# Kernel tuning notes

Hardware: AMD Instinct MI355X
Metric: run time of the kernel (lower is better)

The kernel has to match this reference:

```python
import jax, jax.numpy as jnp
import numpy as np


def _conv(x, w, pad):
    # NCHW conv, stride 1
    return jax.lax.conv_general_dilated(
        x, w, (1, 1), [(pad, pad), (pad, pad)],
        dimension_numbers=('NCHW', 'OIHW', 'NCHW'))


def _bn_relu(x, s, b, m, v):
    # eval-mode BatchNorm2d (running stats) + ReLU, eps=1e-5
    inv = s / jnp.sqrt(v + 1e-5)
    return jax.nn.relu(x * inv[None, :, None, None] + (b - m * inv)[None, :, None, None])


def _pam(x, qw, qb, kw, kb, vw, vb, gamma):
    B, C, H, W = x.shape
    N = H * W
    q = (_conv(x, qw, 0) + qb[None, :, None, None]).reshape(B, -1, N)  # [B,Cr,N]
    k = (_conv(x, kw, 0) + kb[None, :, None, None]).reshape(B, -1, N)  # [B,Cr,N]
    v = (_conv(x, vw, 0) + vb[None, :, None, None]).reshape(B, C, N)   # [B,C,N]
    energy = jnp.einsum('bcn,bcm->bnm', q, k)          # [B,N,N], query n over keys m
    att = jax.nn.softmax(energy, axis=-1)
    out = jnp.einsum('bcm,bnm->bcn', v, att).reshape(B, C, H, W)
    return gamma * out + x


def _cam(x, gamma):
    B, C, H, W = x.shape
    f = x.reshape(B, C, -1)                            # [B,C,N]
    energy = jnp.einsum('bcn,bdn->bcd', f, f)          # [B,C,C]
    energy_new = jnp.max(energy, axis=-1, keepdims=True) - energy
    att = jax.nn.softmax(energy_new, axis=-1)
    out = jnp.einsum('bcd,bdn->bcn', att, f).reshape(B, C, H, W)
    return gamma * out + x


def _forward(x, w5a, bn5a_s, bn5a_b, bn5a_m, bn5a_v,
             pq_w, pq_b, pk_w, pk_b, pv_w, pv_b, p_gamma,
             w51, bn51_s, bn51_b, bn51_m, bn51_v,
             w5c, bn5c_s, bn5c_b, bn5c_m, bn5c_v, c_gamma,
             w52, bn52_s, bn52_b, bn52_m, bn52_v,
             w8, b8):
    feat1 = _bn_relu(_conv(x, w5a, 1), bn5a_s, bn5a_b, bn5a_m, bn5a_v)
    sa_feat = _pam(feat1, pq_w, pq_b, pk_w, pk_b, pv_w, pv_b, p_gamma)
    sa_conv = _bn_relu(_conv(sa_feat, w51, 1), bn51_s, bn51_b, bn51_m, bn51_v)
    feat2 = _bn_relu(_conv(x, w5c, 1), bn5c_s, bn5c_b, bn5c_m, bn5c_v)
    sc_feat = _cam(feat2, c_gamma)
    sc_conv = _bn_relu(_conv(sc_feat, w52, 1), bn52_s, bn52_b, bn52_m, bn52_v)
    feat_sum = sa_conv + sc_conv
    # conv8 = Dropout2d (identity in eval) -> 1x1 conv -> ReLU
    sasc = jax.nn.relu(_conv(feat_sum, w8, 0) + b8[None, :, None, None])
    return sasc


def setup_inputs() -> dict:
    key = jax.random.key(0)
    ks = iter(jax.random.split(key, 48))
    def rn(shape, scale=0.1):
        return jax.random.normal(next(ks), shape, jnp.float32) * scale
    def bn_params(c):
        s = rn((c,), 0.2) + 1.0
        b = rn((c,), 0.1)
        m = rn((c,), 0.1)
        v = jnp.abs(rn((c,), 0.5)) + 0.5
        return s, b, m, v
    Cin, Ci, Cout = 512, 32, 2
    Cr = max(1, Ci // 8)  # = 4
    inp = {}
    inp['x'] = jax.random.normal(next(ks), (4, Cin, 64, 64), jnp.float32)
    inp['w5a'] = rn((Ci, Cin, 3, 3), 0.05)
    inp['bn5a_s'], inp['bn5a_b'], inp['bn5a_m'], inp['bn5a_v'] = bn_params(Ci)
    inp['pq_w'] = rn((Cr, Ci, 1, 1)); inp['pq_b'] = rn((Cr,), 0.01)
    inp['pk_w'] = rn((Cr, Ci, 1, 1)); inp['pk_b'] = rn((Cr,), 0.01)
    inp['pv_w'] = rn((Ci, Ci, 1, 1)); inp['pv_b'] = rn((Ci,), 0.01)
    inp['p_gamma'] = jnp.full((1,), 0.5, jnp.float32)
    inp['w51'] = rn((Ci, Ci, 3, 3))
    inp['bn51_s'], inp['bn51_b'], inp['bn51_m'], inp['bn51_v'] = bn_params(Ci)
    inp['w5c'] = rn((Ci, Cin, 3, 3), 0.05)
    inp['bn5c_s'], inp['bn5c_b'], inp['bn5c_m'], inp['bn5c_v'] = bn_params(Ci)
    inp['c_gamma'] = jnp.full((1,), 0.5, jnp.float32)
    inp['w52'] = rn((Ci, Ci, 3, 3))
    inp['bn52_s'], inp['bn52_b'], inp['bn52_m'], inp['bn52_v'] = bn_params(Ci)
    inp['w8'] = rn((Cout, Ci, 1, 1)); inp['b8'] = rn((Cout,), 0.01)
    return inp


def reference(x, w5a, bn5a_s, bn5a_b, bn5a_m, bn5a_v,
              pq_w, pq_b, pk_w, pk_b, pv_w, pv_b, p_gamma,
              w51, bn51_s, bn51_b, bn51_m, bn51_v,
              w5c, bn5c_s, bn5c_b, bn5c_m, bn5c_v, c_gamma,
              w52, bn52_s, bn52_b, bn52_m, bn52_v,
              w8, b8):
    return _forward(x, w5a, bn5a_s, bn5a_b, bn5a_m, bn5a_v,
                    pq_w, pq_b, pk_w, pk_b, pv_w, pv_b, p_gamma,
                    w51, bn51_s, bn51_b, bn51_m, bn51_v,
                    w5c, bn5c_s, bn5c_b, bn5c_m, bn5c_v, c_gamma,
                    w52, bn52_s, bn52_b, bn52_m, bn52_v,
                    w8, b8)
```

## Files before the change

kernel.cpp:

```cpp
#include <hip/hip_runtime.h>
#include <hip/hip_bf16.h>


typedef __attribute__((ext_vector_type(8))) short bf16x8;
typedef __attribute__((ext_vector_type(4))) float f32x4;

#define O_WPK   0
#define O_W51P  147456
#define O_W52P  152064
#define O_BNA   156672
#define O_W8    156928
#define O_PQW   157000
#define O_PKW   157132
#define O_PVW   157264
#define O_GAM   158320
#define O_Q     158400
#define O_K     223936
#define O_ENE   453312
#define O_PE    457408
#define O_F1T   985792
#define O_F2T   1510080
#define O_V     2034368
#define O_SAT   2558656
#define O_SCT   2837440
#define O_XT    461504
#define O_CP    4922048
#define O_PO    4922048
#define O_PS    3116224

__device__ __forceinline__ unsigned short f2b(float f){
  __hip_bfloat16 h = __float2bfloat16(f);
  return *(unsigned short*)&h;
}

__global__ __launch_bounds__(256) void k_prep_all(
  const float* w5a, const float* w5c,
  const float* w51, const float* w52,
  const float* s0,const float* b0,const float* m0,const float* v0,
  const float* s1,const float* b1,const float* m1,const float* v1,
  const float* s2,const float* b2,const float* m2,const float* v2,
  const float* s3,const float* b3,const float* m3,const float* v3,
  const float* w8,const float* b8,
  const float* pqw,const float* pqb,const float* pkw,const float* pkb,
  const float* pvw,const float* pvb,const float* pg,const float* cg,
  float* ws)
{
  int bx = blockIdx.x;
  int tid = threadIdx.x;
  if (bx < 1152){
    int id = bx*256 + tid;
    int tap = id >> 15;
    int r = id & 32767;
    int cb = r >> 11;
    int r2 = r & 2047;
    int co = r2 >> 5, ci = r2 & 31;
    int cin = cb*32 + ci;
    float v = (co < 32) ? w5a[co*4608 + cin*9 + tap] : w5c[(co-32)*4608 + cin*9 + tap];
    ((unsigned short*)ws)[id] = f2b(v);
    return;
  }
  if (bx < 1231){
    int id = (bx-1152)*256 + tid;
    if (id >= 20076) return;
    if (id < 9216){ int tap=id>>10, co=(id>>5)&31, ci=id&31;
      ((unsigned short*)(ws + O_W51P))[id] = f2b(w51[co*288 + ci*9 + tap]); return; }
    id -= 9216;
    if (id < 9216){ int tap=id>>10, co=(id>>5)&31, ci=id&31;
      ((unsigned short*)(ws + O_W52P))[id] = f2b(w52[co*288 + ci*9 + tap]); return; }
    id -= 9216;
    if (id < 256){
      int conv = id>>6, ab = (id>>5)&1, c = id&31;
      const float *S,*Bb,*M,*V;
      if (conv==0){S=s0;Bb=b0;M=m0;V=v0;} else if (conv==1){S=s1;Bb=b1;M=m1;V=v1;}
      else if (conv==2){S=s2;Bb=b2;M=m2;V=v2;} else {S=s3;Bb=b3;M=m3;V=v3;}
      float A = S[c] * rsqrtf(V[c] + 1e-5f);
      ws[O_BNA + conv*64 + ab*32 + c] = ab ? (Bb[c] - M[c]*A) : A;
      return; }
    id -= 256;
    if (id < 64){ ws[O_W8+id] = w8[id]; return; } id -= 64;
    if (id < 2){ ws[O_W8+64+id] = b8[id]; return; } id -= 2;
    if (id < 128){ ws[O_PQW+id] = pqw[id]; return; } id -= 128;
    if (id < 4){ ws[O_PQW+128+id] = pqb[id]; return; } id -= 4;
    if (id < 128){ ws[O_PKW+id] = pkw[id]; return; } id -= 128;
    if (id < 4){ ws[O_PKW+128+id] = pkb[id]; return; } id -= 4;
    if (id < 1024){ ws[O_PVW+id] = pvw[id]; return; } id -= 1024;
    if (id < 32){ ws[O_PVW+1024+id] = pvb[id]; return; } id -= 32;
    ws[O_GAM+id] = id ? cg[0] : pg[0];
    return;
  }
  {
    int i = (bx-1231)*256 + tid;
    if (i >= 66560) return;
    int part = i & 3; int j = i >> 2;
    int rp = j % 260; int bc = j / 260;
    int py, px;
    if (rp < 66){ py = 0; px = rp; }
    else if (rp < 132){ py = 65; px = rp - 66; }
    else if (rp < 196){ py = rp - 131; px = 0; }
    else { py = rp - 195; px = 65; }
    size_t off = (((size_t)bc*66 + py)*66 + px)*32 + part*8;
    *(uint4*)((unsigned short*)(ws + O_XT) + off) = make_uint4(0,0,0,0);
  }
}

__global__ __launch_bounds__(256) void k_nhwc(const float* __restrict__ x, float* __restrict__ ws){
  int y = blockIdx.x, ct = blockIdx.y, b = blockIdx.z;
  __shared__ unsigned short t16[64][65];
  int tid = threadIdx.x;
  int r0 = tid >> 4, c0 = (tid & 15) * 4;
  const float* xb = x + ((size_t)(b*512 + ct*64))*4096 + y*64;
  #pragma unroll
  for (int i = 0; i < 4; ++i){
    int row = r0 + i*16;
    float4 v = *(const float4*)(xb + (size_t)row*4096 + c0);
    t16[row][c0+0] = f2b(v.x);
    t16[row][c0+1] = f2b(v.y);
    t16[row][c0+2] = f2b(v.z);
    t16[row][c0+3] = f2b(v.w);
  }
  __syncthreads();
  int pixl = tid >> 2, q = tid & 3;
  unsigned short vs[16];
  #pragma unroll
  for (int j = 0; j < 16; ++j) vs[j] = t16[q*16 + j][pixl];
  unsigned u[8];
  #pragma unroll
  for (int j = 0; j < 8; ++j) u[j] = (unsigned)vs[2*j] | ((unsigned)vs[2*j+1] << 16);
  unsigned short* xt = (unsigned short*)(ws + O_XT);
  int cbl = ct*2 + (q>>1);
  size_t off = (((size_t)(b*16 + cbl)*66 + (y+1))*66 + (pixl+1))*32 + (q&1)*16;
  *(uint4*)(xt + off)     = make_uint4(u[0],u[1],u[2],u[3]);
  *(uint4*)(xt + off + 8) = make_uint4(u[4],u[5],u[6],u[7]);
}

__global__ __launch_bounds__(256) void k_conv_mfma(float* __restrict__ ws){
  int mb = blockIdx.x;
  int ks = blockIdx.y;
  int b = mb >> 6, y = mb & 63;
  __shared__ unsigned short Bs[198*40];
  int tid = threadIdx.x;
  int w = tid >> 6, l = tid & 63;
  f32x4 zero = {0.f,0.f,0.f,0.f};
  f32x4 acc[4] = {zero, zero, zero, zero};
  const unsigned short* wp = (const unsigned short*)ws;
  const unsigned short* xt = (const unsigned short*)(ws + O_XT);
  int arow = w*16 + (l & 15);
  int kq = (l >> 4)*8;
  int i0 = tid, i1 = tid + 256, i2 = tid + 512, i3 = tid + 768;
  const unsigned short* slab0 = xt + ((size_t)((b*16 + ks*4)*66 + y))*2112;
  uint4 r0 = *(const uint4*)(slab0 + i0*8);
  uint4 r1 = *(const uint4*)(slab0 + i1*8);
  uint4 r2 = *(const uint4*)(slab0 + i2*8);
  uint4 r3 = (tid < 24) ? *(const uint4*)(slab0 + i3*8) : make_uint4(0,0,0,0);
  for (int cb4 = 0; cb4 < 4; ++cb4){
    int cb = ks*4 + cb4;
    __syncthreads();
    *(uint4*)&Bs[(i0>>2)*40 + (i0&3)*8] = r0;
    *(uint4*)&Bs[(i1>>2)*40 + (i1&3)*8] = r1;
    *(uint4*)&Bs[(i2>>2)*40 + (i2&3)*8] = r2;
    if (tid < 24) *(uint4*)&Bs[(i3>>2)*40 + (i3&3)*8] = r3;
    __syncthreads();
    if (cb4 < 3){
      const unsigned short* slab = xt + ((size_t)((b*16 + cb + 1)*66 + y))*2112;
      r0 = *(const uint4*)(slab + i0*8);
      r1 = *(const uint4*)(slab + i1*8);
      r2 = *(const uint4*)(slab + i2*8);
      if (tid < 24) r3 = *(const uint4*)(slab + i3*8);
    }
    #pragma unroll
    for (int tap = 0; tap < 9; ++tap){
      int dy = tap/3, dx = tap - dy*3;
      bf16x8 af = *(const bf16x8*)(wp + (size_t)(tap*16 + cb)*2048 + arow*32 + kq);
      #pragma unroll
      for (int pt = 0; pt < 4; ++pt){
        int pix = pt*16 + (l&15) + dx;
        bf16x8 bv = *(const bf16x8*)&Bs[(dy*66 + pix)*40 + kq];
        acc[pt] = __builtin_amdgcn_mfma_f32_16x16x32_bf16(af, bv, acc[pt], 0, 0, 0);
      }
    }
  }
  float* cp = ws + O_CP + ((size_t)(ks*4 + b))*262144;
  int co0 = w*16 + (l>>4)*4;
  #pragma unroll
  for (int pt = 0; pt < 4; ++pt){
    int pix = y*64 + pt*16 + (l & 15);
    *(f32x4*)&cp[(size_t)pix*64 + co0] = acc[pt];
  }
}

__global__ __launch_bounds__(256) void k_reduce_feat(float* __restrict__ ws){
  int bx = blockIdx.x;
  if (bx < 4096){
    int id = bx*256 + threadIdx.x;
    float s = (ws[O_CP + id] + ws[O_CP + 1048576 + id])
            + (ws[O_CP + 2097152 + id] + ws[O_CP + 3145728 + id]);
    int co = id & 63; int rest = id >> 6;
    int conv = co >> 5, c = co & 31;
    float A = ws[O_BNA + conv*64 + c], Bb = ws[O_BNA + conv*64 + 32 + c];
    float val = fmaxf(A*s + Bb, 0.f);
    if (conv == 0) ws[O_F1T + (size_t)rest*32 + c] = val;
    else           ws[O_F2T + (size_t)rest*32 + c] = val;
    return;
  }
  {
    int i = (bx-4096)*256 + threadIdx.x;
    if (i >= 8320) return;
    int part = i & 3; int j = i >> 2;
    int arr = j / 1040; int rem = j - arr*1040;
    int b = rem / 260; int rp = rem % 260;
    int py, px;
    if (rp < 66){ py = 0; px = rp; }
    else if (rp < 132){ py = 65; px = rp - 66; }
    else if (rp < 196){ py = rp - 131; px = 0; }
    else { py = rp - 195; px = 65; }
    size_t off = (((size_t)(b*66) + py)*66 + px)*32 + part*8;
    unsigned short* base = (unsigned short*)(ws + O_SAT + arr*278784);
    *(uint4*)(base + off) = make_uint4(0,0,0,0);
  }
}

__global__ __launch_bounds__(256) void k_qkv_came(float* __restrict__ ws){
  int bx = blockIdx.x;
  int tid = threadIdx.x;
  __shared__ float wq[32], wk[32], wv[8][32];
  __shared__ float Fs[64*32];
  if (bx < 256){
    int id = bx*256 + tid;
    int part = id >> 14;
    int nid = id & 16383;
    int b = nid >> 12, n = nid & 4095;
    if (tid < 32){ wq[tid] = ws[O_PQW + part*32 + tid]; wk[tid] = ws[O_PKW + part*32 + tid]; }
    wv[tid>>5][tid&31] = ws[O_PVW + (part*8 + (tid>>5))*32 + (tid&31)];
    __syncthreads();
    const float* fp = ws + O_F1T + (size_t)nid*32;
    float fv[32];
    #pragma unroll
    for (int j=0;j<8;j++){
      float4 v = *(const float4*)(fp + j*4);
      fv[j*4]=v.x; fv[j*4+1]=v.y; fv[j*4+2]=v.z; fv[j*4+3]=v.w;
    }
    float q = ws[O_PQW+128+part], k = ws[O_PKW+128+part];
    #pragma unroll
    for (int c=0;c<32;c++){ q += wq[c]*fv[c]; k += wk[c]*fv[c]; }
    ws[O_Q + (((b<<2)+part)<<12) + n] = q;
    ws[O_K + (((b<<2)+part)<<12) + n] = k;
    unsigned short* vbp = (unsigned short*)(ws + O_V);
    #pragma unroll
    for (int j2=0;j2<8;j2++){
      int c2 = part*8 + j2;
      float v = ws[O_PVW+1024+c2];
      #pragma unroll
      for (int c=0;c<32;c++) v += wv[j2][c]*fv[c];
      vbp[(((b<<5)+c2)<<12) + n] = f2b(v);
    }
    return;
  }
  {
    int blk = bx - 256; int b = blk >> 6, ch = blk & 63;
    const float* f = ws + O_F2T + ((size_t)b<<17) + (size_t)ch*2048;
    for (int i = tid; i < 512; i += 256)
      *(float4*)&Fs[i*4] = *(const float4*)(f + i*4);
    __syncthreads();
    int c = tid >> 3, d0 = (tid & 7) * 4;
    float a0=0.f, a1=0.f, a2=0.f, a3=0.f;
    #pragma unroll 8
    for (int n = 0; n < 64; ++n){
      float fc = Fs[n*32 + c];
      float4 fd = *(const float4*)&Fs[n*32 + d0];
      a0 = fmaf(fc, fd.x, a0); a1 = fmaf(fc, fd.y, a1);
      a2 = fmaf(fc, fd.z, a2); a3 = fmaf(fc, fd.w, a3);
    }
    float* pe = ws + O_PE + ((size_t)(b*64 + ch))*1024;
    *(float4*)&pe[c*32 + d0] = make_float4(a0, a1, a2, a3);
  }
}

__global__ __launch_bounds__(256, 6) void k_pam_flash(float* __restrict__ ws){
  int nt = blockIdx.x;
  int b  = blockIdx.y;
  int ms = blockIdx.z;
  __shared__ float Ks[2][4][4][32];
  __shared__ float Ss[4][32];
  __shared__ float Os[4][32][36];
  int tid = threadIdx.x;
  int w = tid >> 6, l = tid & 63;
  int nn = l & 15, g = l >> 4;
  int n0 = (nt<<5) + nn;
  const float LOG2E = 1.44269504f;
  const float BIAS  = -28.8539008f;
  float q0[4], q1[4];
  #pragma unroll
  for (int cr=0;cr<4;++cr){
    q0[cr] = ws[O_Q + (((b<<2)+cr)<<12) + n0] * LOG2E;
    q1[cr] = ws[O_Q + (((b<<2)+cr)<<12) + n0 + 16] * LOG2E;
  }
  int e0i = l*2, cr_s = e0i >> 5, mm_s = e0i & 31;
  int mbase = ms*1024 + w*256;
  const float* ksrc = ws + O_K + (((b<<2)+cr_s)<<12) + mbase + mm_s;
  const unsigned short* vb = (const unsigned short*)(ws + O_V);
  int mo = g*8;
  const unsigned short* vp0 = vb + (((b<<5) + nn)<<12) + mbase + mo;
  const unsigned short* vp1 = vb + (((b<<5) + 16 + nn)<<12) + mbase + mo;
  f32x4 zero = {0.f,0.f,0.f,0.f};
  f32x4 acc00 = zero, acc01 = zero, acc10 = zero, acc11 = zero;
  float lsum0 = 0.f, lsum1 = 0.f;
  bf16x8 a0A = *(const bf16x8*)(vp0);
  bf16x8 a1A = *(const bf16x8*)(vp1);
  float2 kreg = *(const float2*)(ksrc);
  *(float2*)&Ks[0][w][cr_s][mm_s] = kreg;
  bf16x8 a0B, a1B;
  for (int ch = 0; ch < 8; ++ch){
    int buf = ch & 1;
    if (ch < 7){
      int mn = (ch+1)*32;
      a0B = *(const bf16x8*)(vp0 + mn);
      a1B = *(const bf16x8*)(vp1 + mn);
      kreg = *(const float2*)(ksrc + mn);
    }
    float e0[8], e1[8];
    {
      float4 ka, kb;
      ka = *(const float4*)&Ks[buf][w][0][mo];
      kb = *(const float4*)&Ks[buf][w][0][mo+4];
      e0[0]=fmaf(q0[0],ka.x,BIAS); e0[1]=fmaf(q0[0],ka.y,BIAS); e0[2]=fmaf(q0[0],ka.z,BIAS); e0[3]=fmaf(q0[0],ka.w,BIAS);
      e0[4]=fmaf(q0[0],kb.x,BIAS); e0[5]=fmaf(q0[0],kb.y,BIAS); e0[6]=fmaf(q0[0],kb.z,BIAS); e0[7]=fmaf(q0[0],kb.w,BIAS);
      e1[0]=fmaf(q1[0],ka.x,BIAS); e1[1]=fmaf(q1[0],ka.y,BIAS); e1[2]=fmaf(q1[0],ka.z,BIAS); e1[3]=fmaf(q1[0],ka.w,BIAS);
      e1[4]=fmaf(q1[0],kb.x,BIAS); e1[5]=fmaf(q1[0],kb.y,BIAS); e1[6]=fmaf(q1[0],kb.z,BIAS); e1[7]=fmaf(q1[0],kb.w,BIAS);
#define KACC(CR) \
      ka = *(const float4*)&Ks[buf][w][CR][mo]; \
      kb = *(const float4*)&Ks[buf][w][CR][mo+4]; \
      e0[0]=fmaf(q0[CR],ka.x,e0[0]); e0[1]=fmaf(q0[CR],ka.y,e0[1]); e0[2]=fmaf(q0[CR],ka.z,e0[2]); e0[3]=fmaf(q0[CR],ka.w,e0[3]); \
      e0[4]=fmaf(q0[CR],kb.x,e0[4]); e0[5]=fmaf(q0[CR],kb.y,e0[5]); e0[6]=fmaf(q0[CR],kb.z,e0[6]); e0[7]=fmaf(q0[CR],kb.w,e0[7]); \
      e1[0]=fmaf(q1[CR],ka.x,e1[0]); e1[1]=fmaf(q1[CR],ka.y,e1[1]); e1[2]=fmaf(q1[CR],ka.z,e1[2]); e1[3]=fmaf(q1[CR],ka.w,e1[3]); \
      e1[4]=fmaf(q1[CR],kb.x,e1[4]); e1[5]=fmaf(q1[CR],kb.y,e1[5]); e1[6]=fmaf(q1[CR],kb.z,e1[6]); e1[7]=fmaf(q1[CR],kb.w,e1[7]);
      KACC(1)
      KACC(2)
      KACC(3)
#undef KACC
    }
    union { bf16x8 v; unsigned short u[8]; } pb0, pb1;
    #pragma unroll
    for (int j=0;j<8;j++){ float p = __builtin_amdgcn_exp2f(e0[j]); lsum0 += p; pb0.u[j] = f2b(p); }
    #pragma unroll
    for (int j=0;j<8;j++){ float p = __builtin_amdgcn_exp2f(e1[j]); lsum1 += p; pb1.u[j] = f2b(p); }
    acc00 = __builtin_amdgcn_mfma_f32_16x16x32_bf16(a0A, pb0.v, acc00, 0, 0, 0);
    acc01 = __builtin_amdgcn_mfma_f32_16x16x32_bf16(a1A, pb0.v, acc01, 0, 0, 0);
    acc10 = __builtin_amdgcn_mfma_f32_16x16x32_bf16(a0A, pb1.v, acc10, 0, 0, 0);
    acc11 = __builtin_amdgcn_mfma_f32_16x16x32_bf16(a1A, pb1.v, acc11, 0, 0, 0);
    if (ch < 7){
      int nb = buf ^ 1;
      *(float2*)&Ks[nb][w][cr_s][mm_s] = kreg;
      a0A = a0B; a1A = a1B;
    }
  }
  lsum0 += __shfl_xor(lsum0, 16); lsum0 += __shfl_xor(lsum0, 32);
  lsum1 += __shfl_xor(lsum1, 16); lsum1 += __shfl_xor(lsum1, 32);
  if (l < 16){ Ss[w][l] = lsum0; Ss[w][16+l] = lsum1; }
  #pragma unroll
  for (int r=0;r<4;r++){
    Os[w][nn][g*4 + r]         = acc00[r];
    Os[w][nn][16 + g*4 + r]    = acc01[r];
    Os[w][16+nn][g*4 + r]      = acc10[r];
    Os[w][16+nn][16 + g*4 + r] = acc11[r];
  }
  __syncthreads();
  float* PO = ws + O_PO + (size_t)(ms*4+b)*131072 + nt*1024;
  for (int i = tid; i < 1024; i += 256){
    int nn2 = i >> 5, c = i & 31;
    PO[i] = Os[0][nn2][c] + Os[1][nn2][c] + Os[2][nn2][c] + Os[3][nn2][c];
  }
  if (tid < 32)
    ws[O_PS + (ms*4+b)*4096 + (nt<<5) + tid] = Ss[0][tid]+Ss[1][tid]+Ss[2][tid]+Ss[3][tid];
}

__global__ __launch_bounds__(256) void k_finred(float* __restrict__ ws){
  int bx = blockIdx.x;
  if (bx < 2048){
    int id = bx*256 + threadIdx.x;
    int c = id & 31;
    int n = (id >> 5) & 4095;
    int b = id >> 17;
    int pbase = (b*4096 + n)*32 + c;
    int sbase = b*4096 + n;
    float O = ws[O_PO + pbase] + ws[O_PO + 524288 + pbase]
            + ws[O_PO + 1048576 + pbase] + ws[O_PO + 1572864 + pbase];
    float S = ws[O_PS + sbase] + ws[O_PS + 16384 + sbase]
            + ws[O_PS + 32768 + sbase] + ws[O_PS + 49152 + sbase];
    float sa = ws[O_GAM]*(O/S) + ws[O_F1T + id];
    int y = n >> 6, xx = n & 63;
    ((unsigned short*)(ws + O_SAT))[(((size_t)((b*66 + y+1)*66 + xx+1))<<5) + c] = f2b(sa);
    return;
  }
  {
    int id = (bx-2048)*256 + threadIdx.x;
    int b = id >> 10, i = id & 1023;
    const float* pe = ws + O_PE + ((size_t)b<<16) + i;
    float s = 0.f;
    #pragma unroll 8
    for (int chk = 0; chk < 64; ++chk) s += pe[chk*1024];
    ws[O_ENE + id] = s;
  }
}

__global__ __launch_bounds__(256) void k_cam_out(float* __restrict__ ws){
  int blk = blockIdx.x;
  int b = blk >> 5;
  int chunk = blk & 31;
  int tid = threadIdx.x;
  int half = tid >> 7;
  int nl = tid & 127;
  int n = (chunk << 7) + nl;
  __shared__ float att[32][33];
  if (tid < 32){
    int c = tid;
    const float* e = ws + O_ENE + (b<<10) + (c<<5);
    float M = -1e30f, mn = 1e30f;
    #pragma unroll
    for (int d=0;d<32;d++){ M = fmaxf(M, e[d]); mn = fminf(mn, e[d]); }
    float mx2 = M - mn;
    float s = 0.f, ex[32];
    #pragma unroll
    for (int d=0;d<32;d++){ ex[d] = __expf((M - e[d]) - mx2); s += ex[d]; }
    float inv = 1.f/s;
    #pragma unroll
    for (int d=0;d<32;d++) att[c][d] = ex[d]*inv;
  }
  __syncthreads();
  const float* fp = ws + O_F2T + (((size_t)b<<12) + n)*32;
  float fv[32];
  #pragma unroll
  for (int j=0;j<8;j++){
    float4 v = *(const float4*)(fp + j*4);
    fv[j*4]=v.x; fv[j*4+1]=v.y; fv[j*4+2]=v.z; fv[j*4+3]=v.w;
  }
  float g = ws[O_GAM+1];
  int c0 = half*16;
  unsigned u[8];
  #pragma unroll
  for (int cp=0; cp<8; ++cp){
    int ca = c0 + 2*cp, cb = ca + 1;
    float o0 = 0.f, o1 = 0.f;
    #pragma unroll
    for (int d=0;d<32;d++){ o0 += att[ca][d]*fv[d]; o1 += att[cb][d]*fv[d]; }
    float r0 = g*o0 + fv[ca], r1 = g*o1 + fv[cb];
    u[cp] = (unsigned)f2b(r0) | ((unsigned)f2b(r1) << 16);
  }
  int y = n >> 6, xcol = n & 63;
  unsigned short* sct = (unsigned short*)(ws + O_SCT);
  size_t base = ((size_t)((b*66 + y+1)*66 + xcol+1))*32 + c0;
  *(uint4*)(sct + base)     = make_uint4(u[0],u[1],u[2],u[3]);
  *(uint4*)(sct + base + 8) = make_uint4(u[4],u[5],u[6],u[7]);
}

__global__ __launch_bounds__(256) void k_final_mfma(float* __restrict__ ws, float* __restrict__ out){
  int y = blockIdx.x, b = blockIdx.y;
  __shared__ unsigned short Bs[2*3*66*40];
  __shared__ float ep[2][2][2][16];
  int tid = threadIdx.x;
  int w = tid >> 6, l = tid & 63;
  int g = l >> 4, col = l & 15;
  const unsigned short* sat = (const unsigned short*)(ws + O_SAT);
  const unsigned short* sct = (const unsigned short*)(ws + O_SCT);
  for (int i = tid; i < 1584; i += 256){
    int row = i >> 2, part = i & 3;
    int conv = row / 198; int rr = row - conv*198;
    int dy = rr / 66; int pix = rr - dy*66;
    const unsigned short* src = (conv ? sct : sat) + ((size_t)((b*66 + y + dy)*66 + pix))*32 + part*8;
    *(uint4*)&Bs[(size_t)row*40 + part*8] = *(const uint4*)src;
  }
  __syncthreads();
  int cohalf = w & 1, ptbase = (w >> 1) * 2;
  const unsigned short* wp[2] = { (const unsigned short*)(ws + O_W51P), (const unsigned short*)(ws + O_W52P) };
  f32x4 zero = {0.f,0.f,0.f,0.f};
  f32x4 acc[2][2] = {{zero,zero},{zero,zero}};
  for (int dy = 0; dy < 3; ++dy){
    for (int dx = 0; dx < 3; ++dx){
      int tap = dy*3 + dx;
      #pragma unroll
      for (int conv = 0; conv < 2; ++conv){
        bf16x8 af = *(const bf16x8*)(wp[conv] + tap*1024 + (cohalf*16 + col)*32 + g*8);
        #pragma unroll
        for (int pt = 0; pt < 2; ++pt){
          int pix = (ptbase + pt)*16 + col + dx;
          bf16x8 bv = *(const bf16x8*)&Bs[(size_t)((conv*3 + dy)*66 + pix)*40 + g*8];
          acc[conv][pt] = __builtin_amdgcn_mfma_f32_16x16x32_bf16(af, bv, acc[conv][pt], 0, 0, 0);
        }
      }
    }
  }
  float p0[2], p1[2];
  #pragma unroll
  for (int pt = 0; pt < 2; ++pt){
    float s0 = 0.f, s1 = 0.f;
    #pragma unroll
    for (int r = 0; r < 4; ++r){
      int co = cohalf*16 + g*4 + r;
      float A1 = ws[O_BNA + 2*64 + co], B1 = ws[O_BNA + 2*64 + 32 + co];
      float A2 = ws[O_BNA + 3*64 + co], B2 = ws[O_BNA + 3*64 + 32 + co];
      float fs = fmaxf(A1*acc[0][pt][r] + B1, 0.f) + fmaxf(A2*acc[1][pt][r] + B2, 0.f);
      s0 += ws[O_W8 + co]*fs;
      s1 += ws[O_W8 + 32 + co]*fs;
    }
    s0 += __shfl_xor(s0, 16); s0 += __shfl_xor(s0, 32);
    s1 += __shfl_xor(s1, 16); s1 += __shfl_xor(s1, 32);
    p0[pt] = s0; p1[pt] = s1;
  }
  if (cohalf == 0 && l < 16){
    #pragma unroll
    for (int pt = 0; pt < 2; ++pt){ ep[w>>1][pt][0][l] = p0[pt]; ep[w>>1][pt][1][l] = p1[pt]; }
  }
  __syncthreads();
  if (cohalf == 1 && l < 16){
    float b80 = ws[O_W8 + 64], b81 = ws[O_W8 + 65];
    #pragma unroll
    for (int pt = 0; pt < 2; ++pt){
      int pix = y*64 + (w>>1)*32 + pt*16 + l;
      float o0 = p0[pt] + ep[w>>1][pt][0][l] + b80;
      float o1 = p1[pt] + ep[w>>1][pt][1][l] + b81;
      out[((b*2+0)<<12) + pix] = fmaxf(o0, 0.f);
      out[((b*2+1)<<12) + pix] = fmaxf(o1, 0.f);
    }
  }
}

extern "C" void kernel_launch(void* const* d_in, const int* in_sizes, int n_in,
                              void* d_out, int out_size, void* d_ws, size_t ws_size,
                              hipStream_t stream) {
  const float* x    = (const float*)d_in[0];
  float* ws = (float*)d_ws;
  float* out = (float*)d_out;

  k_prep_all<<<1491, 256, 0, stream>>>(
      (const float*)d_in[1], (const float*)d_in[18],
      (const float*)d_in[13], (const float*)d_in[24],
      (const float*)d_in[2],(const float*)d_in[3],(const float*)d_in[4],(const float*)d_in[5],
      (const float*)d_in[19],(const float*)d_in[20],(const float*)d_in[21],(const float*)d_in[22],
      (const float*)d_in[14],(const float*)d_in[15],(const float*)d_in[16],(const float*)d_in[17],
      (const float*)d_in[25],(const float*)d_in[26],(const float*)d_in[27],(const float*)d_in[28],
      (const float*)d_in[29],(const float*)d_in[30],
      (const float*)d_in[6],(const float*)d_in[7],(const float*)d_in[8],(const float*)d_in[9],
      (const float*)d_in[10],(const float*)d_in[11],(const float*)d_in[12],(const float*)d_in[23],
      ws);
  k_nhwc<<<dim3(64,8,4), 256, 0, stream>>>(x, ws);
  k_conv_mfma<<<dim3(256,4), 256, 0, stream>>>(ws);
  k_reduce_feat<<<4129, 256, 0, stream>>>(ws);
  k_qkv_came<<<512, 256, 0, stream>>>(ws);
  k_pam_flash<<<dim3(128,4,4), 256, 0, stream>>>(ws);
  k_finred<<<2064, 256, 0, stream>>>(ws);
  k_cam_out<<<128, 256, 0, stream>>>(ws);
  k_final_mfma<<<dim3(64,4), 256, 0, stream>>>(ws, out);
}
```

Measured before the change: 96.73 us.

## Fuse NHWC transpose into prep, and fuse split-K reduce with QKV and CAM energy

Merges the input NHWC/bf16 transpose into the weight-prep kernel, which saves one launch. Fuses the split-K conv reduction and BN+ReLU with the PAM q/k/v projection and the CAM Gram-matrix partials, all computed from a shared-memory tile, so the separate QKV/CAM kernel and its re-read of the features go away. It also vectorizes the final PAM reduction with f32x4 loads and packed bf16 stores. The costs are a larger partial-energy buffer (128 chunks instead of 64) and lower occupancy in the fused kernel because only half its threads do the projection.

```diff
diff --git a/kernel.cpp b/kernel.cpp
--- a/kernel.cpp
+++ b/kernel.cpp
@@ -17,7 +17,6 @@
 #define O_Q     158400
 #define O_K     223936
 #define O_ENE   453312
-#define O_PE    457408
 #define O_F1T   985792
 #define O_F2T   1510080
 #define O_V     2034368
@@ -27,13 +26,15 @@
 #define O_CP    4922048
 #define O_PO    4922048
 #define O_PS    3116224
+#define O_PE2   9437184
 
 __device__ __forceinline__ unsigned short f2b(float f){
   __hip_bfloat16 h = __float2bfloat16(f);
   return *(unsigned short*)&h;
 }
 
-__global__ __launch_bounds__(256) void k_prep_all(
+__global__ __launch_bounds__(256) void k_prep_nhwc(
+  const float* __restrict__ x,
   const float* w5a, const float* w5c,
   const float* w51, const float* w52,
   const float* s0,const float* b0,const float* m0,const float* v0,
@@ -47,8 +48,38 @@
 {
   int bx = blockIdx.x;
   int tid = threadIdx.x;
-  if (bx < 1152){
-    int id = bx*256 + tid;
+  __shared__ unsigned short t16[64][65];
+  if (bx < 2048){
+    int y = bx & 63, ct = (bx >> 6) & 7, b = bx >> 9;
+    int r0 = tid >> 4, c0 = (tid & 15) * 4;
+    const float* xb = x + ((size_t)(b*512 + ct*64))*4096 + y*64;
+    #pragma unroll
+    for (int i = 0; i < 4; ++i){
+      int row = r0 + i*16;
+      float4 v = *(const float4*)(xb + (size_t)row*4096 + c0);
+      t16[row][c0+0] = f2b(v.x);
+      t16[row][c0+1] = f2b(v.y);
+      t16[row][c0+2] = f2b(v.z);
+      t16[row][c0+3] = f2b(v.w);
+    }
+    __syncthreads();
+    int pixl = tid >> 2, q = tid & 3;
+    unsigned short vs[16];
+    #pragma unroll
+    for (int j = 0; j < 16; ++j) vs[j] = t16[q*16 + j][pixl];
+    unsigned u[8];
+    #pragma unroll
+    for (int j = 0; j < 8; ++j) u[j] = (unsigned)vs[2*j] | ((unsigned)vs[2*j+1] << 16);
+    unsigned short* xt = (unsigned short*)(ws + O_XT);
+    int cbl = ct*2 + (q>>1);
+    size_t off = (((size_t)(b*16 + cbl)*66 + (y+1))*66 + (pixl+1))*32 + (q&1)*16;
+    *(uint4*)(xt + off)     = make_uint4(u[0],u[1],u[2],u[3]);
+    *(uint4*)(xt + off + 8) = make_uint4(u[4],u[5],u[6],u[7]);
+    return;
+  }
+  int pbx = bx - 2048;
+  if (pbx < 1152){
+    int id = pbx*256 + tid;
     int tap = id >> 15;
     int r = id & 32767;
     int cb = r >> 11;
@@ -59,8 +90,8 @@
     ((unsigned short*)ws)[id] = f2b(v);
     return;
   }
-  if (bx < 1231){
-    int id = (bx-1152)*256 + tid;
+  if (pbx < 1231){
+    int id = (pbx-1152)*256 + tid;
     if (id >= 20076) return;
     if (id < 9216){ int tap=id>>10, co=(id>>5)&31, ci=id&31;
       ((unsigned short*)(ws + O_W51P))[id] = f2b(w51[co*288 + ci*9 + tap]); return; }
@@ -89,7 +120,7 @@
     return;
   }
   {
-    int i = (bx-1231)*256 + tid;
+    int i = (pbx-1231)*256 + tid;
     if (i >= 66560) return;
     int part = i & 3; int j = i >> 2;
     int rp = j % 260; int bc = j / 260;
@@ -101,36 +132,6 @@
     size_t off = (((size_t)bc*66 + py)*66 + px)*32 + part*8;
     *(uint4*)((unsigned short*)(ws + O_XT) + off) = make_uint4(0,0,0,0);
   }
-}
-
-__global__ __launch_bounds__(256) void k_nhwc(const float* __restrict__ x, float* __restrict__ ws){
-  int y = blockIdx.x, ct = blockIdx.y, b = blockIdx.z;
-  __shared__ unsigned short t16[64][65];
-  int tid = threadIdx.x;
-  int r0 = tid >> 4, c0 = (tid & 15) * 4;
-  const float* xb = x + ((size_t)(b*512 + ct*64))*4096 + y*64;
-  #pragma unroll
-  for (int i = 0; i < 4; ++i){
-    int row = r0 + i*16;
-    float4 v = *(const float4*)(xb + (size_t)row*4096 + c0);
-    t16[row][c0+0] = f2b(v.x);
-    t16[row][c0+1] = f2b(v.y);
-    t16[row][c0+2] = f2b(v.z);
-    t16[row][c0+3] = f2b(v.w);
-  }
-  __syncthreads();
-  int pixl = tid >> 2, q = tid & 3;
-  unsigned short vs[16];
-  #pragma unroll
-  for (int j = 0; j < 16; ++j) vs[j] = t16[q*16 + j][pixl];
-  unsigned u[8];
-  #pragma unroll
-  for (int j = 0; j < 8; ++j) u[j] = (unsigned)vs[2*j] | ((unsigned)vs[2*j+1] << 16);
-  unsigned short* xt = (unsigned short*)(ws + O_XT);
-  int cbl = ct*2 + (q>>1);
-  size_t off = (((size_t)(b*16 + cbl)*66 + (y+1))*66 + (pixl+1))*32 + (q&1)*16;
-  *(uint4*)(xt + off)     = make_uint4(u[0],u[1],u[2],u[3]);
-  *(uint4*)(xt + off + 8) = make_uint4(u[4],u[5],u[6],u[7]);
 }
 
 __global__ __launch_bounds__(256) void k_conv_mfma(float* __restrict__ ws){
@@ -188,22 +189,88 @@
   }
 }
 
-__global__ __launch_bounds__(256) void k_reduce_feat(float* __restrict__ ws){
+__global__ __launch_bounds__(256) void k_feat(float* __restrict__ ws){
   int bx = blockIdx.x;
-  if (bx < 4096){
-    int id = bx*256 + threadIdx.x;
-    float s = (ws[O_CP + id] + ws[O_CP + 1048576 + id])
-            + (ws[O_CP + 2097152 + id] + ws[O_CP + 3145728 + id]);
-    int co = id & 63; int rest = id >> 6;
-    int conv = co >> 5, c = co & 31;
-    float A = ws[O_BNA + conv*64 + c], Bb = ws[O_BNA + conv*64 + 32 + c];
-    float val = fmaxf(A*s + Bb, 0.f);
-    if (conv == 0) ws[O_F1T + (size_t)rest*32 + c] = val;
-    else           ws[O_F2T + (size_t)rest*32 + c] = val;
+  int tid = threadIdx.x;
+  __shared__ float Fl[32][68];
+  __shared__ float wqs[4][32], wks[4][32], wvs[32][32];
+  if (bx < 512){
+    int b = bx >> 7, chunk = bx & 127;
+    for (int i = tid; i < 1280; i += 256){
+      if (i < 128)      ((float*)wqs)[i]     = ws[O_PQW + i];
+      else if (i < 256) ((float*)wks)[i-128] = ws[O_PKW + (i-128)];
+      else              ((float*)wvs)[i-256] = ws[O_PVW + (i-256)];
+    }
+    int pix = tid >> 3, cg = tid & 7;
+    int pixg = (chunk << 5) + pix;
+    const float* cpb = ws + O_CP + (size_t)b*262144 + (size_t)pixg*64 + cg*8;
+    f32x4 sa_ = *(const f32x4*)(cpb);
+    f32x4 sb_ = *(const f32x4*)(cpb + 4);
+    {
+      f32x4 t0 = *(const f32x4*)(cpb + 1048576);
+      f32x4 t1 = *(const f32x4*)(cpb + 1048576 + 4);
+      f32x4 t2 = *(const f32x4*)(cpb + 2097152);
+      f32x4 t3 = *(const f32x4*)(cpb + 2097152 + 4);
+      f32x4 t4 = *(const f32x4*)(cpb + 3145728);
+      f32x4 t5 = *(const f32x4*)(cpb + 3145728 + 4);
+      sa_ = (sa_ + t0) + (t2 + t4);
+      sb_ = (sb_ + t1) + (t3 + t5);
+    }
+    int co0 = cg*8;
+    int conv = co0 >> 5, cc0 = co0 & 31;
+    float v8[8];
+    #pragma unroll
+    for (int j = 0; j < 8; ++j){
+      int c = cc0 + j;
+      float A = ws[O_BNA + conv*64 + c], Bb = ws[O_BNA + conv*64 + 32 + c];
+      float s = (j < 4) ? sa_[j] : sb_[j-4];
+      v8[j] = fmaxf(A*s + Bb, 0.f);
+    }
+    float* fdst = ws + (conv == 0 ? O_F1T : O_F2T) + ((size_t)(b*4096 + pixg))*32 + cc0;
+    *(f32x4*)(fdst)     = (f32x4){v8[0],v8[1],v8[2],v8[3]};
+    *(f32x4*)(fdst + 4) = (f32x4){v8[4],v8[5],v8[6],v8[7]};
+    *(f32x4*)&Fl[pix][co0]     = (f32x4){v8[0],v8[1],v8[2],v8[3]};
+    *(f32x4*)&Fl[pix][co0 + 4] = (f32x4){v8[4],v8[5],v8[6],v8[7]};
+    __syncthreads();
+    if (tid < 128){
+      int part = tid >> 5, pixl = tid & 31;
+      int n = (chunk << 5) + pixl;
+      float fv[32];
+      #pragma unroll
+      for (int c = 0; c < 32; ++c) fv[c] = Fl[pixl][c];
+      float q = ws[O_PQW+128+part], k = ws[O_PKW+128+part];
+      #pragma unroll
+      for (int c = 0; c < 32; ++c){ q += wqs[part][c]*fv[c]; k += wks[part][c]*fv[c]; }
+      ws[O_Q + (((b<<2)+part)<<12) + n] = q;
+      ws[O_K + (((b<<2)+part)<<12) + n] = k;
+      unsigned short* vbp = (unsigned short*)(ws + O_V);
+      #pragma unroll
+      for (int j2 = 0; j2 < 8; ++j2){
+        int c2 = part*8 + j2;
+        float v = ws[O_PVW+1024+c2];
+        #pragma unroll
+        for (int c = 0; c < 32; ++c) v += wvs[c2][c]*fv[c];
+        vbp[(((b<<5)+c2)<<12) + n] = f2b(v);
+      }
+    }
+    {
+      int ce = tid >> 3, d0 = (tid & 7) * 4;
+      float a0=0.f, a1=0.f, a2=0.f, a3=0.f;
+      #pragma unroll 8
+      for (int n = 0; n < 32; ++n){
+        float fc = Fl[n][32 + ce];
+        float f0 = Fl[n][32 + d0], f1 = Fl[n][32 + d0 + 1];
+        float f2 = Fl[n][32 + d0 + 2], f3 = Fl[n][32 + d0 + 3];
+        a0 = fmaf(fc, f0, a0); a1 = fmaf(fc, f1, a1);
+        a2 = fmaf(fc, f2, a2); a3 = fmaf(fc, f3, a3);
+      }
+      float* pe = ws + O_PE2 + ((size_t)(b*128 + chunk))*1024 + ce*32 + d0;
+      *(f32x4*)pe = (f32x4){a0, a1, a2, a3};
+    }
     return;
   }
   {
-    int i = (bx-4096)*256 + threadIdx.x;
+    int i = (bx-512)*256 + tid;
     if (i >= 8320) return;
     int part = i & 3; int j = i >> 2;
     int arr = j / 1040; int rem = j - arr*1040;
@@ -216,62 +283,6 @@
     size_t off = (((size_t)(b*66) + py)*66 + px)*32 + part*8;
     unsigned short* base = (unsigned short*)(ws + O_SAT + arr*278784);
     *(uint4*)(base + off) = make_uint4(0,0,0,0);
-  }
-}
-
-__global__ __launch_bounds__(256) void k_qkv_came(float* __restrict__ ws){
-  int bx = blockIdx.x;
-  int tid = threadIdx.x;
-  __shared__ float wq[32], wk[32], wv[8][32];
-  __shared__ float Fs[64*32];
-  if (bx < 256){
-    int id = bx*256 + tid;
-    int part = id >> 14;
-    int nid = id & 16383;
-    int b = nid >> 12, n = nid & 4095;
-    if (tid < 32){ wq[tid] = ws[O_PQW + part*32 + tid]; wk[tid] = ws[O_PKW + part*32 + tid]; }
-    wv[tid>>5][tid&31] = ws[O_PVW + (part*8 + (tid>>5))*32 + (tid&31)];
-    __syncthreads();
-    const float* fp = ws + O_F1T + (size_t)nid*32;
-    float fv[32];
-    #pragma unroll
-    for (int j=0;j<8;j++){
-      float4 v = *(const float4*)(fp + j*4);
-      fv[j*4]=v.x; fv[j*4+1]=v.y; fv[j*4+2]=v.z; fv[j*4+3]=v.w;
-    }
-    float q = ws[O_PQW+128+part], k = ws[O_PKW+128+part];
-    #pragma unroll
-    for (int c=0;c<32;c++){ q += wq[c]*fv[c]; k += wk[c]*fv[c]; }
-    ws[O_Q + (((b<<2)+part)<<12) + n] = q;
-    ws[O_K + (((b<<2)+part)<<12) + n] = k;
-    unsigned short* vbp = (unsigned short*)(ws + O_V);
-    #pragma unroll
-    for (int j2=0;j2<8;j2++){
-      int c2 = part*8 + j2;
-      float v = ws[O_PVW+1024+c2];
-      #pragma unroll
-      for (int c=0;c<32;c++) v += wv[j2][c]*fv[c];
-      vbp[(((b<<5)+c2)<<12) + n] = f2b(v);
-    }
-    return;
-  }
-  {
-    int blk = bx - 256; int b = blk >> 6, ch = blk & 63;
-    const float* f = ws + O_F2T + ((size_t)b<<17) + (size_t)ch*2048;
-    for (int i = tid; i < 512; i += 256)
-      *(float4*)&Fs[i*4] = *(const float4*)(f + i*4);
-    __syncthreads();
-    int c = tid >> 3, d0 = (tid & 7) * 4;
-    float a0=0.f, a1=0.f, a2=0.f, a3=0.f;
-    #pragma unroll 8
-    for (int n = 0; n < 64; ++n){
-      float fc = Fs[n*32 + c];
-      float4 fd = *(const float4*)&Fs[n*32 + d0];
-      a0 = fmaf(fc, fd.x, a0); a1 = fmaf(fc, fd.y, a1);
-      a2 = fmaf(fc, fd.z, a2); a3 = fmaf(fc, fd.w, a3);
-    }
-    float* pe = ws + O_PE + ((size_t)(b*64 + ch))*1024;
-    *(float4*)&pe[c*32 + d0] = make_float4(a0, a1, a2, a3);
   }
 }
 
@@ -375,29 +386,39 @@
 
 __global__ __launch_bounds__(256) void k_finred(float* __restrict__ ws){
   int bx = blockIdx.x;
-  if (bx < 2048){
-    int id = bx*256 + threadIdx.x;
-    int c = id & 31;
-    int n = (id >> 5) & 4095;
-    int b = id >> 17;
-    int pbase = (b*4096 + n)*32 + c;
+  int tid = threadIdx.x;
+  if (bx < 512){
+    int id = bx*256 + tid;
+    int cq = (id & 7) * 4;
+    int n  = (id >> 3) & 4095;
+    int b  = id >> 15;
+    size_t pbase = (size_t)(b*4096 + n)*32 + cq;
     int sbase = b*4096 + n;
-    float O = ws[O_PO + pbase] + ws[O_PO + 524288 + pbase]
-            + ws[O_PO + 1048576 + pbase] + ws[O_PO + 1572864 + pbase];
+    f32x4 O = *(const f32x4*)(ws + O_PO + pbase);
+    O = O + *(const f32x4*)(ws + O_PO + 524288 + pbase);
+    O = O + *(const f32x4*)(ws + O_PO + 1048576 + pbase);
+    O = O + *(const f32x4*)(ws + O_PO + 1572864 + pbase);
     float S = ws[O_PS + sbase] + ws[O_PS + 16384 + sbase]
             + ws[O_PS + 32768 + sbase] + ws[O_PS + 49152 + sbase];
-    float sa = ws[O_GAM]*(O/S) + ws[O_F1T + id];
+    float gam = ws[O_GAM];
+    f32x4 f1 = *(const f32x4*)(ws + O_F1T + (size_t)id*4);
+    unsigned short h[4];
+    #pragma unroll
+    for (int j = 0; j < 4; ++j) h[j] = f2b(gam*(O[j]/S) + f1[j]);
     int y = n >> 6, xx = n & 63;
-    ((unsigned short*)(ws + O_SAT))[(((size_t)((b*66 + y+1)*66 + xx+1))<<5) + c] = f2b(sa);
+    unsigned short* sat = (unsigned short*)(ws + O_SAT);
+    uint2 u; u.x = (unsigned)h[0] | ((unsigned)h[1] << 16);
+             u.y = (unsigned)h[2] | ((unsigned)h[3] << 16);
+    *(uint2*)&sat[(((size_t)((b*66 + y+1)*66 + xx+1))<<5) + cq] = u;
     return;
   }
   {
-    int id = (bx-2048)*256 + threadIdx.x;
+    int id = (bx-512)*256 + tid;
     int b = id >> 10, i = id & 1023;
-    const float* pe = ws + O_PE + ((size_t)b<<16) + i;
+    const float* pe = ws + O_PE2 + ((size_t)b)*131072 + i;
     float s = 0.f;
     #pragma unroll 8
-    for (int chk = 0; chk < 64; ++chk) s += pe[chk*1024];
+    for (int chk = 0; chk < 128; ++chk) s += pe[chk*1024];
     ws[O_ENE + id] = s;
   }
 }
@@ -530,7 +551,8 @@
   float* ws = (float*)d_ws;
   float* out = (float*)d_out;
 
-  k_prep_all<<<1491, 256, 0, stream>>>(
+  k_prep_nhwc<<<3539, 256, 0, stream>>>(
+      x,
       (const float*)d_in[1], (const float*)d_in[18],
       (const float*)d_in[13], (const float*)d_in[24],
       (const float*)d_in[2],(const float*)d_in[3],(const float*)d_in[4],(const float*)d_in[5],
@@ -541,12 +563,10 @@
       (const float*)d_in[6],(const float*)d_in[7],(const float*)d_in[8],(const float*)d_in[9],
       (const float*)d_in[10],(const float*)d_in[11],(const float*)d_in[12],(const float*)d_in[23],
       ws);
-  k_nhwc<<<dim3(64,8,4), 256, 0, stream>>>(x, ws);
   k_conv_mfma<<<dim3(256,4), 256, 0, stream>>>(ws);
-  k_reduce_feat<<<4129, 256, 0, stream>>>(ws);
-  k_qkv_came<<<512, 256, 0, stream>>>(ws);
+  k_feat<<<545, 256, 0, stream>>>(ws);
   k_pam_flash<<<dim3(128,4,4), 256, 0, stream>>>(ws);
-  k_finred<<<2064, 256, 0, stream>>>(ws);
+  k_finred<<<528, 256, 0, stream>>>(ws);
   k_cam_out<<<128, 256, 0, stream>>>(ws);
   k_final_mfma<<<dim3(64,4), 256, 0, stream>>>(ws, out);
 }
```

New measurement: 95.26 us. About the same (-1.5%).
